# Kernel optimization log

Hardware: AMD Instinct MI355X
Metric: run time of the kernel (lower is better)

Reference implementation:

```python
import jax, jax.numpy as jnp
import numpy as np

N_EMBED = 2048
N_HEAD = 16
N_KV_HEAD = 4
HEAD_DIM = N_EMBED // N_HEAD
REPEAT = N_HEAD // N_KV_HEAD
THETA = 10000.0


def setup_inputs() -> dict:
    key = jax.random.key(0)
    ks = jax.random.split(key, 9)
    B, T = 2, 2048
    s = 0.02
    return {
        'x': jax.random.normal(ks[0], (B, T, N_EMBED), jnp.float32),
        'Wq': jax.random.normal(ks[1], (N_EMBED, N_EMBED), jnp.float32) * s,
        'bq': jax.random.normal(ks[2], (N_EMBED,), jnp.float32) * s,
        'Wk': jax.random.normal(ks[3], (N_EMBED, N_KV_HEAD * HEAD_DIM), jnp.float32) * s,
        'bk': jax.random.normal(ks[4], (N_KV_HEAD * HEAD_DIM,), jnp.float32) * s,
        'Wv': jax.random.normal(ks[5], (N_EMBED, N_KV_HEAD * HEAD_DIM), jnp.float32) * s,
        'bv': jax.random.normal(ks[6], (N_KV_HEAD * HEAD_DIM,), jnp.float32) * s,
        'Wo': jax.random.normal(ks[7], (N_EMBED, N_EMBED), jnp.float32) * s,
        'bo': jax.random.normal(ks[8], (N_EMBED,), jnp.float32) * s,
    }


def _rope_angles(T):
    # Quirk of original: freqs exponent uses full n_embed, then sliced to head_dim//2
    freqs = THETA ** (-(jnp.arange(0, N_EMBED, 2, dtype=jnp.float32) / N_EMBED))
    freqs = freqs[: HEAD_DIM // 2]
    t = jnp.arange(T, dtype=jnp.float32)
    return jnp.outer(t, freqs)  # [T, HEAD_DIM//2]


def _apply_rope(x, cos, sin):
    # x: [B, T, H, D]; pairs are adjacent elements along D
    xr = x[..., 0::2]
    xi = x[..., 1::2]
    # cos/sin: [1, T, 1, D//2]
    or_ = xr * cos - xi * sin
    oi_ = xr * sin + xi * cos
    out = jnp.stack([or_, oi_], axis=-1).reshape(x.shape)
    # original casts rope output to bfloat16
    return out.astype(jnp.bfloat16).astype(jnp.float32)


def reference(x, Wq, bq, Wk, bk, Wv, bv, Wo, bo):
    B, T, _ = x.shape
    q = (x @ Wq + bq).reshape(B, T, N_HEAD, HEAD_DIM)
    k = (x @ Wk + bk).reshape(B, T, N_KV_HEAD, HEAD_DIM)
    v = (x @ Wv + bv).reshape(B, T, N_KV_HEAD, HEAD_DIM)

    ang = _rope_angles(T)
    cos = jnp.cos(ang)[None, :, None, :]
    sin = jnp.sin(ang)[None, :, None, :]
    xq = _apply_rope(q, cos, sin)
    xk = _apply_rope(k, cos, sin)

    xq = xq.transpose(0, 2, 1, 3)                 # [B, H, T, D]
    xk = xk.transpose(0, 2, 1, 3)                 # [B, Hkv, T, D]
    xv = v.transpose(0, 2, 1, 3)                  # [B, Hkv, T, D]
    xk = jnp.repeat(xk, REPEAT, axis=1)           # [B, H, T, D]
    xv = jnp.repeat(xv, REPEAT, axis=1)

    qk = jnp.einsum('bhtd,bhsd->bhts', xq, xk)    # [B, H, T, T]
    causal = jnp.tril(jnp.ones((T, T), dtype=bool))
    qk = jnp.where(causal[None, None], qk, -jnp.inf)
    # Quirk: scale applied AFTER softmax, using n_embed**-0.5
    attn = jax.nn.softmax(qk, axis=-1) * (N_EMBED ** -0.5)
    o = jnp.einsum('bhts,bhsd->bhtd', attn, xv)
    o = o.transpose(0, 2, 1, 3).reshape(B, T, N_EMBED)
    return o @ Wo + bo
```

## Files before the change

### kernel.cpp

```cpp
#include <hip/hip_runtime.h>
#include <stdint.h>
#include <math.h>

typedef unsigned short u16;
typedef __attribute__((ext_vector_type(8))) short short8;
typedef __attribute__((ext_vector_type(8))) _Float16 half8;
typedef __attribute__((ext_vector_type(4))) float float4v;
typedef __attribute__((ext_vector_type(16))) float float16v;
typedef __attribute__((ext_vector_type(4))) u16 ushort4v;

#define T_SEQ 2048
#define NB 2
#define NE 2048
#define NH 16
#define NKV 4
#define HD 128
#define KDIM 2048

union Frag { short8 s; half8 h; };

__device__ inline u16 f32_bf16(float f) {
    union { float f; uint32_t u; } v; v.f = f;
    uint32_t u = v.u;
    return (u16)((u + 0x7fffu + ((u >> 16) & 1u)) >> 16);
}
__device__ inline u16 f32_f16(float f) {
    union { _Float16 h; u16 u; } v; v.h = (_Float16)f;
    return v.u;
}

typedef __attribute__((address_space(1))) const void g_void;
typedef __attribute__((address_space(3))) void l_void;
#define GLOAD16(g, l) __builtin_amdgcn_global_load_lds((g_void*)(g), (l_void*)(l), 16, 0, 0)

__global__ void conv_f16(const float* __restrict__ in, u16* __restrict__ out) {
    int i = blockIdx.x * blockDim.x + threadIdx.x;
    float4 v = ((const float4*)in)[i];
    ushort4v o;
    o.x = f32_f16(v.x); o.y = f32_f16(v.y); o.z = f32_f16(v.z); o.w = f32_f16(v.w);
    *(ushort4v*)(out + (size_t)i * 4) = o;
}

template<bool TO_F16>
__global__ void transpose_convert(const float* __restrict__ in, u16* __restrict__ out,
                                  int K, int N) {
    __shared__ float tile[32][33];
    int n0 = blockIdx.x * 32, k0 = blockIdx.y * 32;
    int tx = threadIdx.x, ty = threadIdx.y;
    for (int i = 0; i < 32; i += 8)
        tile[ty + i][tx] = in[(size_t)(k0 + ty + i) * N + n0 + tx];
    __syncthreads();
    for (int i = 0; i < 32; i += 8) {
        float v = tile[tx][ty + i];
        out[(size_t)(n0 + ty + i) * K + k0 + tx] = TO_F16 ? f32_f16(v) : f32_bf16(v);
    }
}

__global__ void rope_tab(float* __restrict__ ctab, float* __restrict__ stab) {
    int i = blockIdx.x * blockDim.x + threadIdx.x;
    int t = i >> 6, j = i & 63;
    float freqf = (float)pow(10000.0, -(double)j / 1024.0);
    float angf = (float)t * freqf;
    double a = (double)angf;
    ctab[i] = (float)cos(a);
    stab[i] = (float)sin(a);
}

#define GEMM_STAGE_DECL(Asrc, Bsrc) \
    int rin = lane >> 2, ksl = lane & 3; \
    int u0r = wid * 32; \
    const u16* Ag0 = (Asrc) + (size_t)(m0 + u0r + rin) * KDIM + ksl * 8; \
    const u16* Ag1 = (Asrc) + (size_t)(m0 + u0r + 16 + rin) * KDIM + ksl * 8; \
    const u16* Bg0 = (Bsrc) + (size_t)(n0 + u0r + rin) * KDIM + ksl * 8; \
    const u16* Bg1 = (Bsrc) + (size_t)(n0 + u0r + 16 + rin) * KDIM + ksl * 8; \
    u16* Al0 = &Alds[u0r * 32]; \
    u16* Al1 = &Alds[(u0r + 16) * 32]; \
    u16* Bl0 = &Blds[u0r * 32]; \
    u16* Bl1 = &Blds[(u0r + 16) * 32];

#define GEMM_MAINLOOP(F16) \
    for (int k0 = 0; k0 < KDIM; k0 += 32) { \
        __syncthreads(); \
        GLOAD16(Ag0 + k0, Al0); \
        GLOAD16(Ag1 + k0, Al1); \
        GLOAD16(Bg0 + k0, Bl0); \
        GLOAD16(Bg1 + k0, Bl1); \
        __syncthreads(); \
        Frag af[4], bf[4]; \
        for (int i = 0; i < 4; i++) \
            af[i].s = *(const short8*)&Alds[(wr * 64 + i * 16 + l16) * 32 + quad * 8]; \
        for (int j = 0; j < 4; j++) \
            bf[j].s = *(const short8*)&Blds[(wc * 64 + j * 16 + l16) * 32 + quad * 8]; \
        for (int i = 0; i < 4; i++) \
            for (int j = 0; j < 4; j++) { \
                if (F16) \
                    acc[i][j] = __builtin_amdgcn_mfma_f32_16x16x32_f16(af[i].h, bf[j].h, acc[i][j], 0, 0, 0); \
                else \
                    acc[i][j] = __builtin_amdgcn_mfma_f32_16x16x32_bf16(af[i].s, bf[j].s, acc[i][j], 0, 0, 0); \
            } \
    }

template<int MODE, bool F16IN>
__global__ __launch_bounds__(256)
void gemm_bt(const u16* __restrict__ A, const u16* __restrict__ Bt,
             const float* __restrict__ bias,
             u16* __restrict__ outU, float* __restrict__ outF,
             const float* __restrict__ ctab, const float* __restrict__ stab) {
    __shared__ u16 Alds[128 * 32];
    __shared__ u16 Blds[128 * 32];
    int tid = threadIdx.x;
    int wid = tid >> 6, lane = tid & 63;
    int quad = lane >> 4, l16 = lane & 15;
    int wr = wid >> 1, wc = wid & 1;
    int m0 = blockIdx.x * 128, n0 = blockIdx.y * 128;

    float4v acc[4][4];
    for (int i = 0; i < 4; i++) for (int j = 0; j < 4; j++) acc[i][j] = (float4v){0,0,0,0};

    GEMM_STAGE_DECL(A, Bt)
    GEMM_MAINLOOP(F16IN)

    for (int i = 0; i < 4; i++) {
        int mbase = m0 + wr * 64 + i * 16 + quad * 4;
        for (int j = 0; j < 4; j++) {
            int col = n0 + wc * 64 + j * 16 + l16;
            float bcol = bias[col];
            for (int r = 0; r < 4; r++) {
                int m = mbase + r;
                float val = acc[i][j][r] + bcol;
                if (MODE == 3) {
                    outF[(size_t)m * NE + col] = val;
                } else {
                    int b = m >> 11, t = m & 2047;
                    int h = col >> 7, d = col & 127;
                    int jj = d >> 1;
                    float c = ctab[t * 64 + jj];
                    float s = stab[t * 64 + jj];
                    float partner = __shfl_xor(val, 1, 64);
                    float o = (d & 1) ? (partner * s + val * c) : (val * c - partner * s);
                    outU[(((size_t)(b * NH + h)) * T_SEQ + t) * HD + d] = f32_bf16(o);
                }
            }
        }
    }
}

__global__ __launch_bounds__(256)
void gemm_kv(const u16* __restrict__ xh, const u16* __restrict__ Bk, const u16* __restrict__ Bv,
             const float* __restrict__ bkb, const float* __restrict__ bvb,
             u16* __restrict__ kout, u16* __restrict__ vout,
             const float* __restrict__ ctab, const float* __restrict__ stab) {
    __shared__ u16 Alds[128 * 32];
    __shared__ u16 Blds[128 * 32];
    int tid = threadIdx.x;
    int wid = tid >> 6, lane = tid & 63;
    int quad = lane >> 4, l16 = lane & 15;
    int wr = wid >> 1, wc = wid & 1;
    int which = blockIdx.z;
    int m0, n0;
    const u16* A; const u16* Bt;
    if (which) {
        m0 = blockIdx.y * 128;
        n0 = blockIdx.x * 128;
        A = Bv; Bt = xh;
    } else {
        m0 = blockIdx.x * 128;
        n0 = blockIdx.y * 128;
        A = xh; Bt = Bk;
    }

    float4v acc[4][4];
    for (int i = 0; i < 4; i++) for (int j = 0; j < 4; j++) acc[i][j] = (float4v){0,0,0,0};

    GEMM_STAGE_DECL(A, Bt)
    GEMM_MAINLOOP(true)

    if (which) {
        for (int i = 0; i < 4; i++) {
            int mbase = m0 + wr * 64 + i * 16 + quad * 4;
            float brow[4];
            for (int r = 0; r < 4; r++) brow[r] = bvb[mbase + r];
            for (int j = 0; j < 4; j++) {
                int col = n0 + wc * 64 + j * 16 + l16;
                int b = col >> 11, t = col & 2047;
                for (int r = 0; r < 4; r++) {
                    int m = mbase + r;
                    float val = acc[i][j][r] + brow[r];
                    vout[(((size_t)(b * NKV + (m >> 7))) * HD + (m & 127)) * T_SEQ + t] = f32_bf16(val);
                }
            }
        }
    } else {
        for (int i = 0; i < 4; i++) {
            int mbase = m0 + wr * 64 + i * 16 + quad * 4;
            for (int j = 0; j < 4; j++) {
                int col = n0 + wc * 64 + j * 16 + l16;
                float bcol = bkb[col];
                for (int r = 0; r < 4; r++) {
                    int m = mbase + r;
                    float val = acc[i][j][r] + bcol;
                    int b = m >> 11, t = m & 2047;
                    int h = col >> 7, d = col & 127;
                    int jj = d >> 1;
                    float c = ctab[t * 64 + jj];
                    float s = stab[t * 64 + jj];
                    float partner = __shfl_xor(val, 1, 64);
                    float o = (d & 1) ? (partner * s + val * c) : (val * c - partner * s);
                    kout[(((size_t)(b * NKV + h)) * T_SEQ + t) * HD + d] = f32_bf16(o);
                }
            }
        }
    }
}

__global__ __launch_bounds__(256, 2)
void attn_kernel(const u16* __restrict__ Qr, const u16* __restrict__ Kr,
                 const u16* __restrict__ Vt, u16* __restrict__ Oout) {
    __shared__ u16 smem[27136];
    u16* klds = smem;
    u16* vlds = smem + 8704;
    u16* plds = smem + 17920;
    int tid = threadIdx.x;
    int wid = tid >> 6, lane = tid & 63;
    int l32 = lane & 31, hh = lane >> 5;

    int lin = blockIdx.x + (blockIdx.y << 4);
    int g = lin >> 5, bh = lin & 31;
    int qt = (lin < 256) ? (15 - g) : (g - 8);
    int b = bh >> 4, hd = bh & 15, kvh = hd >> 2;
    int t0 = qt * 128;

    const u16* Qb = Qr + (((size_t)(b * NH + hd)) * T_SEQ + t0 + wid * 32) * HD;
    const u16* Kb = Kr + ((size_t)(b * NKV + kvh)) * T_SEQ * HD;
    const u16* Vb = Vt + ((size_t)(b * NKV + kvh)) * HD * T_SEQ;

    short8 qf[8];
#pragma unroll
    for (int ks = 0; ks < 8; ks++)
        qf[ks] = *(const short8*)(Qb + (size_t)l32 * HD + ks * 16 + hh * 8);

    float16v oacc[4];
#pragma unroll
    for (int dt = 0; dt < 4; dt++)
        oacc[dt] = (float16v){0,0,0,0,0,0,0,0,0,0,0,0,0,0,0,0};
    float m_run = -INFINITY, l_run = 0.f;

    int ksr = tid >> 2, kc = (tid & 3) * 32;
    int vdr = tid >> 1, vc = (tid & 1) * 32;
    u16* pw = plds + wid * 32 * 72;

    int nst = 2 * qt + 2;

    {
        const u16* ksrc = Kb + (size_t)ksr * HD + kc;
        const u16* vsrc = Vb + (size_t)vdr * T_SEQ + vc;
        short8 kr0[4], vr0[4];
#pragma unroll
        for (int i = 0; i < 4; i++) kr0[i] = *(const short8*)(ksrc + i * 8);
#pragma unroll
        for (int i = 0; i < 4; i++) vr0[i] = *(const short8*)(vsrc + i * 8);
#pragma unroll
        for (int i = 0; i < 4; i++) *(short8*)&klds[ksr * 136 + kc + i * 8] = kr0[i];
#pragma unroll
        for (int i = 0; i < 4; i++) *(short8*)&vlds[vdr * 72 + vc + i * 8] = vr0[i];
    }
    __syncthreads();

    for (int st = 0; st < nst; st++) {
        short8 krg[4], vrg[4];
        bool more = (st + 1 < nst);
        if (more) {
            const u16* ksrc = Kb + ((size_t)(st + 1) * 64 + ksr) * HD + kc;
            const u16* vsrc = Vb + (size_t)vdr * T_SEQ + (st + 1) * 64 + vc;
#pragma unroll
            for (int i = 0; i < 4; i++) krg[i] = *(const short8*)(ksrc + i * 8);
#pragma unroll
            for (int i = 0; i < 4; i++) vrg[i] = *(const short8*)(vsrc + i * 8);
        }

        float16v sfa[2];
        sfa[0] = (float16v){0,0,0,0,0,0,0,0,0,0,0,0,0,0,0,0};
        sfa[1] = (float16v){0,0,0,0,0,0,0,0,0,0,0,0,0,0,0,0};
#pragma unroll
        for (int ks = 0; ks < 8; ks++) {
            short8 kf0 = *(const short8*)&klds[l32 * 136 + ks * 16 + hh * 8];
            short8 kf1 = *(const short8*)&klds[(32 + l32) * 136 + ks * 16 + hh * 8];
            sfa[0] = __builtin_amdgcn_mfma_f32_32x32x16_bf16(kf0, qf[ks], sfa[0], 0, 0, 0);
            sfa[1] = __builtin_amdgcn_mfma_f32_32x32x16_bf16(kf1, qf[ks], sfa[1], 0, 0, 0);
        }

        int tg = t0 + wid * 32 + l32;
        if (st >= 2 * qt) {
#pragma unroll
            for (int stile = 0; stile < 2; stile++)
#pragma unroll
                for (int r = 0; r < 16; r++) {
                    int s = st * 64 + stile * 32 + (r & 3) + 8 * (r >> 2) + 4 * hh;
                    if (s > tg) sfa[stile][r] = -INFINITY;
                }
        }

        float mx = -INFINITY;
#pragma unroll
        for (int stile = 0; stile < 2; stile++)
#pragma unroll
            for (int r = 0; r < 16; r++) mx = fmaxf(mx, sfa[stile][r]);
        mx = fmaxf(mx, __shfl_xor(mx, 32, 64));
        float mnew = fmaxf(m_run, mx);
        float alpha = __expf(m_run - mnew);
        float psum = 0.f;
#pragma unroll
        for (int stile = 0; stile < 2; stile++)
#pragma unroll
            for (int r = 0; r < 16; r++) {
                float p = __expf(sfa[stile][r] - mnew);
                sfa[stile][r] = p;
                psum += p;
            }
        psum += __shfl_xor(psum, 32, 64);
        l_run = l_run * alpha + psum;
        m_run = mnew;

#pragma unroll
        for (int stile = 0; stile < 2; stile++)
#pragma unroll
            for (int gq = 0; gq < 4; gq++) {
                ushort4v pk;
                pk.x = f32_bf16(sfa[stile][gq * 4 + 0]);
                pk.y = f32_bf16(sfa[stile][gq * 4 + 1]);
                pk.z = f32_bf16(sfa[stile][gq * 4 + 2]);
                pk.w = f32_bf16(sfa[stile][gq * 4 + 3]);
                *(ushort4v*)&pw[l32 * 72 + stile * 32 + gq * 8 + hh * 4] = pk;
            }

        __syncthreads();

#pragma unroll
        for (int dt = 0; dt < 4; dt++)
#pragma unroll
            for (int r = 0; r < 16; r++) oacc[dt][r] *= alpha;

#pragma unroll
        for (int ks2 = 0; ks2 < 4; ks2++) {
            short8 pf = *(const short8*)&pw[l32 * 72 + ks2 * 16 + hh * 8];
#pragma unroll
            for (int dt = 0; dt < 4; dt++) {
                short8 vf = *(const short8*)&vlds[(dt * 32 + l32) * 72 + ks2 * 16 + hh * 8];
                oacc[dt] = __builtin_amdgcn_mfma_f32_32x32x16_bf16(vf, pf, oacc[dt], 0, 0, 0);
            }
        }

        __syncthreads();
        if (more) {
#pragma unroll
            for (int i = 0; i < 4; i++) *(short8*)&klds[ksr * 136 + kc + i * 8] = krg[i];
#pragma unroll
            for (int i = 0; i < 4; i++) *(short8*)&vlds[vdr * 72 + vc + i * 8] = vrg[i];
        }
        __syncthreads();
    }

    const float scale = 0.022097086912079608f;
    float sc = scale / l_run;
    u16* ow = smem + wid * 4352;
#pragma unroll
    for (int dt = 0; dt < 4; dt++)
#pragma unroll
        for (int gq = 0; gq < 4; gq++) {
            ushort4v pk;
            pk.x = f32_bf16(oacc[dt][gq * 4 + 0] * sc);
            pk.y = f32_bf16(oacc[dt][gq * 4 + 1] * sc);
            pk.z = f32_bf16(oacc[dt][gq * 4 + 2] * sc);
            pk.w = f32_bf16(oacc[dt][gq * 4 + 3] * sc);
            *(ushort4v*)&ow[l32 * 136 + dt * 32 + gq * 8 + hh * 4] = pk;
        }
    __syncthreads();
    int tl = lane >> 4, dcol = (lane & 15) * 8;
#pragma unroll
    for (int ch = 0; ch < 8; ch++) {
        int t_local = tl + ch * 4;
        short8 ov = *(const short8*)&ow[t_local * 136 + dcol];
        *(short8*)&Oout[((size_t)(b * T_SEQ) + t0 + wid * 32 + t_local) * NE + hd * HD + dcol] = ov;
    }
}

extern "C" void kernel_launch(void* const* d_in, const int* in_sizes, int n_in,
                              void* d_out, int out_size, void* d_ws, size_t ws_size,
                              hipStream_t stream) {
    const float* x  = (const float*)d_in[0];
    const float* Wq = (const float*)d_in[1];
    const float* bq = (const float*)d_in[2];
    const float* Wk = (const float*)d_in[3];
    const float* bk = (const float*)d_in[4];
    const float* Wv = (const float*)d_in[5];
    const float* bv = (const float*)d_in[6];
    const float* Wo = (const float*)d_in[7];
    const float* bo = (const float*)d_in[8];
    float* out = (float*)d_out;
    char* ws = (char*)d_ws;

    u16* xh   = (u16*)(ws);
    u16* wqt  = (u16*)(ws + 16777216);
    u16* wkt  = (u16*)(ws + 25165824);
    u16* wvt  = (u16*)(ws + 27262976);
    u16* qr   = (u16*)(ws + 29360128);
    u16* kr   = (u16*)(ws + 46137344);
    u16* vt   = (u16*)(ws + 50331648);
    float* ctab = (float*)(ws + 54525952);
    float* stab = (float*)(ws + 55050240);
    u16* ao  = xh;
    u16* wot = wqt;

    conv_f16<<<8192, 256, 0, stream>>>(x, xh);
    transpose_convert<true><<<dim3(64, 64), dim3(32, 8), 0, stream>>>(Wq, wqt, 2048, 2048);
    transpose_convert<true><<<dim3(16, 64), dim3(32, 8), 0, stream>>>(Wk, wkt, 2048, 512);
    transpose_convert<true><<<dim3(16, 64), dim3(32, 8), 0, stream>>>(Wv, wvt, 2048, 512);
    rope_tab<<<512, 256, 0, stream>>>(ctab, stab);

    gemm_bt<0, true><<<dim3(32, 16), 256, 0, stream>>>(xh, wqt, bq, qr, nullptr, ctab, stab);
    gemm_kv<<<dim3(32, 4, 2), 256, 0, stream>>>(xh, wkt, wvt, bk, bv, kr, vt, ctab, stab);

    transpose_convert<false><<<dim3(64, 64), dim3(32, 8), 0, stream>>>(Wo, wot, 2048, 2048);

    attn_kernel<<<dim3(16, 32), 256, 0, stream>>>(qr, kr, vt, ao);

    gemm_bt<3, false><<<dim3(32, 16), 256, 0, stream>>>(ao, wot, bo, nullptr, out, ctab, stab);
}
```

Measured before the change: 347.8 us.

## Merge QKV GEMMs into one launch and keep attention probabilities in registers

Combines the Q and KV projection GEMMs into a single 768-block launch. In the attention kernel, P is no longer staged through LDS. It is packed with v_cvt_pk_bf16 and permlane32 swaps so it can feed the PV MFMA directly, which removes an LDS round-trip and a barrier and lowers shared memory use. The change also skips fully masked causal tiles per wave, skips the rescale when the running max grows by at most 8 (a lazy rescale), and raises wave priority around the MFMA blocks. The lazy rescale lets exponentials exceed 1, which adds a small bf16 precision risk.

```diff
diff --git a/kernel.cpp b/kernel.cpp
--- a/kernel.cpp
+++ b/kernel.cpp
@@ -27,6 +27,15 @@
 __device__ inline u16 f32_f16(float f) {
     union { _Float16 h; u16 u; } v; v.h = (_Float16)f;
     return v.u;
+}
+
+__device__ inline uint32_t cvtpk_bf16(float lo, float hi) {
+    uint32_t r;
+    asm("v_cvt_pk_bf16_f32 %0, %1, %2" : "=v"(r) : "v"(lo), "v"(hi));
+    return r;
+}
+__device__ inline void perm32swap(uint32_t& a, uint32_t& b) {
+    asm("v_permlane32_swap_b32 %0, %1" : "+v"(a), "+v"(b));
 }
 
 typedef __attribute__((address_space(1))) const void g_void;
@@ -100,86 +109,44 @@
             } \
     }
 
-template<int MODE, bool F16IN>
 __global__ __launch_bounds__(256)
-void gemm_bt(const u16* __restrict__ A, const u16* __restrict__ Bt,
-             const float* __restrict__ bias,
-             u16* __restrict__ outU, float* __restrict__ outF,
-             const float* __restrict__ ctab, const float* __restrict__ stab) {
+void gemm_qkv(const u16* __restrict__ xh, const u16* __restrict__ wqt,
+              const u16* __restrict__ wkt, const u16* __restrict__ wvt,
+              const float* __restrict__ bq, const float* __restrict__ bk,
+              const float* __restrict__ bv,
+              u16* __restrict__ qout, u16* __restrict__ kout, u16* __restrict__ vout,
+              const float* __restrict__ ctab, const float* __restrict__ stab) {
     __shared__ u16 Alds[128 * 32];
     __shared__ u16 Blds[128 * 32];
     int tid = threadIdx.x;
     int wid = tid >> 6, lane = tid & 63;
     int quad = lane >> 4, l16 = lane & 15;
     int wr = wid >> 1, wc = wid & 1;
-    int m0 = blockIdx.x * 128, n0 = blockIdx.y * 128;
+
+    int lin = blockIdx.x;
+    int mode, m0, n0;
+    const u16 *A, *Bt;
+    if (lin < 512) {
+        mode = 0; m0 = (lin >> 4) * 128; n0 = (lin & 15) * 128; A = xh; Bt = wqt;
+    } else if (lin < 640) {
+        int i = lin - 512;
+        mode = 1; m0 = (i >> 2) * 128; n0 = (i & 3) * 128; A = xh; Bt = wkt;
+    } else {
+        int i = lin - 640;
+        mode = 2; m0 = (i & 3) * 128; n0 = (i >> 2) * 128; A = wvt; Bt = xh;
+    }
 
     float4v acc[4][4];
     for (int i = 0; i < 4; i++) for (int j = 0; j < 4; j++) acc[i][j] = (float4v){0,0,0,0};
 
     GEMM_STAGE_DECL(A, Bt)
-    GEMM_MAINLOOP(F16IN)
-
-    for (int i = 0; i < 4; i++) {
-        int mbase = m0 + wr * 64 + i * 16 + quad * 4;
-        for (int j = 0; j < 4; j++) {
-            int col = n0 + wc * 64 + j * 16 + l16;
-            float bcol = bias[col];
-            for (int r = 0; r < 4; r++) {
-                int m = mbase + r;
-                float val = acc[i][j][r] + bcol;
-                if (MODE == 3) {
-                    outF[(size_t)m * NE + col] = val;
-                } else {
-                    int b = m >> 11, t = m & 2047;
-                    int h = col >> 7, d = col & 127;
-                    int jj = d >> 1;
-                    float c = ctab[t * 64 + jj];
-                    float s = stab[t * 64 + jj];
-                    float partner = __shfl_xor(val, 1, 64);
-                    float o = (d & 1) ? (partner * s + val * c) : (val * c - partner * s);
-                    outU[(((size_t)(b * NH + h)) * T_SEQ + t) * HD + d] = f32_bf16(o);
-                }
-            }
-        }
-    }
-}
-
-__global__ __launch_bounds__(256)
-void gemm_kv(const u16* __restrict__ xh, const u16* __restrict__ Bk, const u16* __restrict__ Bv,
-             const float* __restrict__ bkb, const float* __restrict__ bvb,
-             u16* __restrict__ kout, u16* __restrict__ vout,
-             const float* __restrict__ ctab, const float* __restrict__ stab) {
-    __shared__ u16 Alds[128 * 32];
-    __shared__ u16 Blds[128 * 32];
-    int tid = threadIdx.x;
-    int wid = tid >> 6, lane = tid & 63;
-    int quad = lane >> 4, l16 = lane & 15;
-    int wr = wid >> 1, wc = wid & 1;
-    int which = blockIdx.z;
-    int m0, n0;
-    const u16* A; const u16* Bt;
-    if (which) {
-        m0 = blockIdx.y * 128;
-        n0 = blockIdx.x * 128;
-        A = Bv; Bt = xh;
-    } else {
-        m0 = blockIdx.x * 128;
-        n0 = blockIdx.y * 128;
-        A = xh; Bt = Bk;
-    }
-
-    float4v acc[4][4];
-    for (int i = 0; i < 4; i++) for (int j = 0; j < 4; j++) acc[i][j] = (float4v){0,0,0,0};
-
-    GEMM_STAGE_DECL(A, Bt)
     GEMM_MAINLOOP(true)
 
-    if (which) {
+    if (mode == 2) {
         for (int i = 0; i < 4; i++) {
             int mbase = m0 + wr * 64 + i * 16 + quad * 4;
             float brow[4];
-            for (int r = 0; r < 4; r++) brow[r] = bvb[mbase + r];
+            for (int r = 0; r < 4; r++) brow[r] = bv[mbase + r];
             for (int j = 0; j < 4; j++) {
                 int col = n0 + wc * 64 + j * 16 + l16;
                 int b = col >> 11, t = col & 2047;
@@ -191,11 +158,14 @@
             }
         }
     } else {
+        const float* bias = mode ? bk : bq;
+        u16* outU = mode ? kout : qout;
+        int nheads = mode ? NKV : NH;
         for (int i = 0; i < 4; i++) {
             int mbase = m0 + wr * 64 + i * 16 + quad * 4;
             for (int j = 0; j < 4; j++) {
                 int col = n0 + wc * 64 + j * 16 + l16;
-                float bcol = bkb[col];
+                float bcol = bias[col];
                 for (int r = 0; r < 4; r++) {
                     int m = mbase + r;
                     float val = acc[i][j][r] + bcol;
@@ -206,9 +176,37 @@
                     float s = stab[t * 64 + jj];
                     float partner = __shfl_xor(val, 1, 64);
                     float o = (d & 1) ? (partner * s + val * c) : (val * c - partner * s);
-                    kout[(((size_t)(b * NKV + h)) * T_SEQ + t) * HD + d] = f32_bf16(o);
+                    outU[(((size_t)(b * nheads + h)) * T_SEQ + t) * HD + d] = f32_bf16(o);
                 }
             }
+        }
+    }
+}
+
+__global__ __launch_bounds__(256)
+void gemm_out(const u16* __restrict__ A, const u16* __restrict__ Bt,
+              const float* __restrict__ bias, float* __restrict__ outF) {
+    __shared__ u16 Alds[128 * 32];
+    __shared__ u16 Blds[128 * 32];
+    int tid = threadIdx.x;
+    int wid = tid >> 6, lane = tid & 63;
+    int quad = lane >> 4, l16 = lane & 15;
+    int wr = wid >> 1, wc = wid & 1;
+    int m0 = blockIdx.x * 128, n0 = blockIdx.y * 128;
+
+    float4v acc[4][4];
+    for (int i = 0; i < 4; i++) for (int j = 0; j < 4; j++) acc[i][j] = (float4v){0,0,0,0};
+
+    GEMM_STAGE_DECL(A, Bt)
+    GEMM_MAINLOOP(false)
+
+    for (int i = 0; i < 4; i++) {
+        int mbase = m0 + wr * 64 + i * 16 + quad * 4;
+        for (int j = 0; j < 4; j++) {
+            int col = n0 + wc * 64 + j * 16 + l16;
+            float bcol = bias[col];
+            for (int r = 0; r < 4; r++)
+                outF[(size_t)(mbase + r) * NE + col] = acc[i][j][r] + bcol;
         }
     }
 }
@@ -216,10 +214,9 @@
 __global__ __launch_bounds__(256, 2)
 void attn_kernel(const u16* __restrict__ Qr, const u16* __restrict__ Kr,
                  const u16* __restrict__ Vt, u16* __restrict__ Oout) {
-    __shared__ u16 smem[27136];
+    __shared__ u16 smem[17920];
     u16* klds = smem;
     u16* vlds = smem + 8704;
-    u16* plds = smem + 17920;
     int tid = threadIdx.x;
     int wid = tid >> 6, lane = tid & 63;
     int l32 = lane & 31, hh = lane >> 5;
@@ -247,7 +244,6 @@
 
     int ksr = tid >> 2, kc = (tid & 3) * 32;
     int vdr = tid >> 1, vc = (tid & 1) * 32;
-    u16* pw = plds + wid * 32 * 72;
 
     int nst = 2 * qt + 2;
 
@@ -278,76 +274,80 @@
             for (int i = 0; i < 4; i++) vrg[i] = *(const short8*)(vsrc + i * 8);
         }
 
-        float16v sfa[2];
-        sfa[0] = (float16v){0,0,0,0,0,0,0,0,0,0,0,0,0,0,0,0};
-        sfa[1] = (float16v){0,0,0,0,0,0,0,0,0,0,0,0,0,0,0,0};
-#pragma unroll
-        for (int ks = 0; ks < 8; ks++) {
-            short8 kf0 = *(const short8*)&klds[l32 * 136 + ks * 16 + hh * 8];
-            short8 kf1 = *(const short8*)&klds[(32 + l32) * 136 + ks * 16 + hh * 8];
-            sfa[0] = __builtin_amdgcn_mfma_f32_32x32x16_bf16(kf0, qf[ks], sfa[0], 0, 0, 0);
-            sfa[1] = __builtin_amdgcn_mfma_f32_32x32x16_bf16(kf1, qf[ks], sfa[1], 0, 0, 0);
-        }
-
-        int tg = t0 + wid * 32 + l32;
-        if (st >= 2 * qt) {
+        bool active = (st * 64) <= (t0 + wid * 32 + 31);
+        if (active) {
+            float16v sfa[2];
+            sfa[0] = (float16v){0,0,0,0,0,0,0,0,0,0,0,0,0,0,0,0};
+            sfa[1] = (float16v){0,0,0,0,0,0,0,0,0,0,0,0,0,0,0,0};
+            __builtin_amdgcn_s_setprio(1);
+#pragma unroll
+            for (int ks = 0; ks < 8; ks++) {
+                short8 kf0 = *(const short8*)&klds[l32 * 136 + ks * 16 + hh * 8];
+                short8 kf1 = *(const short8*)&klds[(32 + l32) * 136 + ks * 16 + hh * 8];
+                sfa[0] = __builtin_amdgcn_mfma_f32_32x32x16_bf16(kf0, qf[ks], sfa[0], 0, 0, 0);
+                sfa[1] = __builtin_amdgcn_mfma_f32_32x32x16_bf16(kf1, qf[ks], sfa[1], 0, 0, 0);
+            }
+            __builtin_amdgcn_s_setprio(0);
+
+            int tg = t0 + wid * 32 + l32;
+            if (st >= 2 * qt) {
+#pragma unroll
+                for (int stile = 0; stile < 2; stile++)
+#pragma unroll
+                    for (int r = 0; r < 16; r++) {
+                        int s = st * 64 + stile * 32 + (r & 3) + 8 * (r >> 2) + 4 * hh;
+                        if (s > tg) sfa[stile][r] = -INFINITY;
+                    }
+            }
+
+            float mx = -INFINITY;
 #pragma unroll
             for (int stile = 0; stile < 2; stile++)
 #pragma unroll
+                for (int r = 0; r < 16; r++) mx = fmaxf(mx, sfa[stile][r]);
+            mx = fmaxf(mx, __shfl_xor(mx, 32, 64));
+            bool nos = __all(mx - m_run <= 8.f);
+            float mnew = nos ? m_run : fmaxf(m_run, mx);
+            float alpha = nos ? 1.f : __expf(m_run - mnew);
+            float psum = 0.f;
+#pragma unroll
+            for (int stile = 0; stile < 2; stile++)
+#pragma unroll
                 for (int r = 0; r < 16; r++) {
-                    int s = st * 64 + stile * 32 + (r & 3) + 8 * (r >> 2) + 4 * hh;
-                    if (s > tg) sfa[stile][r] = -INFINITY;
+                    float p = __expf(sfa[stile][r] - mnew);
+                    sfa[stile][r] = p;
+                    psum += p;
                 }
-        }
-
-        float mx = -INFINITY;
-#pragma unroll
-        for (int stile = 0; stile < 2; stile++)
-#pragma unroll
-            for (int r = 0; r < 16; r++) mx = fmaxf(mx, sfa[stile][r]);
-        mx = fmaxf(mx, __shfl_xor(mx, 32, 64));
-        float mnew = fmaxf(m_run, mx);
-        float alpha = __expf(m_run - mnew);
-        float psum = 0.f;
-#pragma unroll
-        for (int stile = 0; stile < 2; stile++)
-#pragma unroll
-            for (int r = 0; r < 16; r++) {
-                float p = __expf(sfa[stile][r] - mnew);
-                sfa[stile][r] = p;
-                psum += p;
-            }
-        psum += __shfl_xor(psum, 32, 64);
-        l_run = l_run * alpha + psum;
-        m_run = mnew;
-
-#pragma unroll
-        for (int stile = 0; stile < 2; stile++)
-#pragma unroll
-            for (int gq = 0; gq < 4; gq++) {
-                ushort4v pk;
-                pk.x = f32_bf16(sfa[stile][gq * 4 + 0]);
-                pk.y = f32_bf16(sfa[stile][gq * 4 + 1]);
-                pk.z = f32_bf16(sfa[stile][gq * 4 + 2]);
-                pk.w = f32_bf16(sfa[stile][gq * 4 + 3]);
-                *(ushort4v*)&pw[l32 * 72 + stile * 32 + gq * 8 + hh * 4] = pk;
-            }
-
-        __syncthreads();
-
-#pragma unroll
-        for (int dt = 0; dt < 4; dt++)
-#pragma unroll
-            for (int r = 0; r < 16; r++) oacc[dt][r] *= alpha;
-
-#pragma unroll
-        for (int ks2 = 0; ks2 < 4; ks2++) {
-            short8 pf = *(const short8*)&pw[l32 * 72 + ks2 * 16 + hh * 8];
-#pragma unroll
-            for (int dt = 0; dt < 4; dt++) {
-                short8 vf = *(const short8*)&vlds[(dt * 32 + l32) * 72 + ks2 * 16 + hh * 8];
-                oacc[dt] = __builtin_amdgcn_mfma_f32_32x32x16_bf16(vf, pf, oacc[dt], 0, 0, 0);
-            }
+            psum += __shfl_xor(psum, 32, 64);
+            l_run = l_run * alpha + psum;
+            m_run = mnew;
+
+            if (!nos) {
+#pragma unroll
+                for (int dt = 0; dt < 4; dt++)
+#pragma unroll
+                    for (int r = 0; r < 16; r++) oacc[dt][r] *= alpha;
+            }
+
+            __builtin_amdgcn_s_setprio(1);
+#pragma unroll
+            for (int g2 = 0; g2 < 4; g2++) {
+                int stile = g2 >> 1, gg = g2 & 1;
+                uint32_t P0 = cvtpk_bf16(sfa[stile][8 * gg + 0], sfa[stile][8 * gg + 1]);
+                uint32_t P1 = cvtpk_bf16(sfa[stile][8 * gg + 2], sfa[stile][8 * gg + 3]);
+                uint32_t P2 = cvtpk_bf16(sfa[stile][8 * gg + 4], sfa[stile][8 * gg + 5]);
+                uint32_t P3 = cvtpk_bf16(sfa[stile][8 * gg + 6], sfa[stile][8 * gg + 7]);
+                perm32swap(P0, P2);
+                perm32swap(P1, P3);
+                union { uint32_t w[4]; short8 s; } pf;
+                pf.w[0] = P0; pf.w[1] = P1; pf.w[2] = P2; pf.w[3] = P3;
+#pragma unroll
+                for (int dt = 0; dt < 4; dt++) {
+                    short8 vf = *(const short8*)&vlds[(dt * 32 + l32) * 72 + g2 * 16 + hh * 8];
+                    oacc[dt] = __builtin_amdgcn_mfma_f32_32x32x16_bf16(vf, pf.s, oacc[dt], 0, 0, 0);
+                }
+            }
+            __builtin_amdgcn_s_setprio(0);
         }
 
         __syncthreads();
@@ -417,12 +417,12 @@
     transpose_convert<true><<<dim3(16, 64), dim3(32, 8), 0, stream>>>(Wv, wvt, 2048, 512);
     rope_tab<<<512, 256, 0, stream>>>(ctab, stab);
 
-    gemm_bt<0, true><<<dim3(32, 16), 256, 0, stream>>>(xh, wqt, bq, qr, nullptr, ctab, stab);
-    gemm_kv<<<dim3(32, 4, 2), 256, 0, stream>>>(xh, wkt, wvt, bk, bv, kr, vt, ctab, stab);
+    gemm_qkv<<<dim3(768), 256, 0, stream>>>(xh, wqt, wkt, wvt, bq, bk, bv,
+                                            qr, kr, vt, ctab, stab);
 
     transpose_convert<false><<<dim3(64, 64), dim3(32, 8), 0, stream>>>(Wo, wot, 2048, 2048);
 
     attn_kernel<<<dim3(16, 32), 256, 0, stream>>>(qr, kr, vt, ao);
 
-    gemm_bt<3, false><<<dim3(32, 16), 256, 0, stream>>>(ao, wot, bo, nullptr, out, ctab, stab);
-}
+    gemm_out<<<dim3(32, 16), 256, 0, stream>>>(ao, wot, bo, out);
+}
```

Result: faster. 337.3 us (-3.0%).
